# Kernel tuning notes

Measured on AMD Instinct MI355X. Metric: run time of the kernel, lower is better.

The kernel has to match this reference:

```python
import jax, jax.numpy as jnp
import numpy as np

B, NSL, DS = 8, 12, 768
L, R, DL = 24, 64, 4096
DP = 4096
DIM_T = NSL * 2 * DS          # 18432
FUSED = 1024 + 512            # 1536
GEN_IN = FUSED + 256 + 64     # 1856


def setup_inputs() -> dict:
    key = jax.random.key(0)
    ks = jax.random.split(key, 16)
    s = lambda d: 1.0 / np.sqrt(d)
    return {
        "A_small": jax.random.normal(ks[0], (B, NSL, 1, DS), jnp.float32),
        "B_small": jax.random.normal(ks[1], (B, NSL, DS, 1), jnp.float32),
        "prompt_emb": jax.random.normal(ks[2], (B, DP), jnp.float32),
        "W_ct": jax.random.normal(ks[3], (DIM_T, 1024), jnp.float32) * s(DIM_T),
        "b_ct": jnp.zeros((1024,), jnp.float32),
        "W_cp": jax.random.normal(ks[4], (DP, 512), jnp.float32) * s(DP),
        "b_cp": jnp.zeros((512,), jnp.float32),
        "W_pc": jax.random.normal(ks[5], (FUSED, L), jnp.float32) * s(FUSED),
        "b_pc": jnp.zeros((L,), jnp.float32),
        "E_layer": jax.random.normal(ks[6], (L, 256), jnp.float32),
        "E_chunk": jax.random.normal(ks[7], (R, 64), jnp.float32),
        "W_A": jax.random.normal(ks[8], (GEN_IN, DL), jnp.float32) * s(GEN_IN),
        "b_A": jnp.zeros((DL,), jnp.float32),
        "W_B": jax.random.normal(ks[9], (GEN_IN, DL), jnp.float32) * s(GEN_IN),
        "b_B": jnp.zeros((DL,), jnp.float32),
    }


def reference(A_small, B_small, prompt_emb, W_ct, b_ct, W_cp, b_cp, W_pc, b_pc,
              E_layer, E_chunk, W_A, b_A, W_B, b_B):
    bsz = prompt_emb.shape[0]
    flat_T = jnp.concatenate([A_small.reshape(bsz, -1), B_small.reshape(bsz, -1)], axis=-1)
    t_feat = jax.nn.relu(flat_T @ W_ct + b_ct)          # [B,1024]
    p_feat = jax.nn.relu(prompt_emb @ W_cp + b_cp)      # [B,512]
    fused = jnp.concatenate([t_feat, p_feat], axis=-1)  # [B,1536]
    logits = fused @ W_pc + b_pc                        # [B,L]
    y_soft = jax.nn.sigmoid(logits)                     # eval mode (no gumbel)
    y_hard = (y_soft > 0.5).astype(y_soft.dtype)
    gate = y_soft + jax.lax.stop_gradient(y_hard - y_soft)  # straight-through

    # Batched hypernetwork over all (layer, chunk) pairs instead of a double loop.
    ctx = jnp.broadcast_to(fused[:, None, None, :], (bsz, L, R, FUSED))
    le = jnp.broadcast_to(E_layer[None, :, None, :], (bsz, L, R, 256))
    ce = jnp.broadcast_to(E_chunk[None, None, :, :], (bsz, L, R, 64))
    gen = jnp.concatenate([ctx, le, ce], axis=-1)       # [B,L,R,1856]

    A = gen @ W_A + b_A                                 # [B,L,R,DL]
    Bm = gen @ W_B + b_B                                # [B,L,R,DL]
    A_large = A * gate[:, :, None, None]                # [B,L,R,DL]
    B_large = jnp.transpose(Bm, (0, 1, 3, 2))           # [B,L,DL,R]
    return (A_large, B_large, gate)
```

## Files before the change

kernel.cpp:

```cpp
#include <hip/hip_runtime.h>

typedef float v4f __attribute__((ext_vector_type(4)));

#define NB 8
#define NL 24
#define NR 64
#define ND 4096
#define NFUSED 1536
#define NTF 1024
#define NPF 512
#define KP 4096

#define FKC 12

#define WS_FACC  0
#define WS_GATE  49152
#define WS_PLA   49344
#define WS_PLB   245952
#define WS_CA    442560
#define WS_CBT   704704
#define WS_PFA   966848
#define WS_PFB   1360064

__global__ __launch_bounds__(256) void k_indep(
    const float* __restrict__ As, const float* __restrict__ Bs,
    const float* __restrict__ W_ct,
    const float* __restrict__ prompt, const float* __restrict__ W_cp,
    const float* __restrict__ E_layer, const float* __restrict__ E_chunk,
    const float* __restrict__ W_A, const float* __restrict__ W_B,
    float* __restrict__ fAcc,
    float* __restrict__ pLA, float* __restrict__ pLB,
    float* __restrict__ CA, float* __restrict__ CBT) {
  __shared__ float e[NR * 64];
  const int bx = blockIdx.x;
  const int tid = threadIdx.x;

  if (bx < 576) {
    const int j = (bx & 3) * 256 + tid;
    const int kc = bx >> 2;
    const int kbase = kc * 128;
    const float* xsrc = (kbase < 9216) ? (As + kbase) : (Bs + (kbase - 9216));
    {
      const int i0 = tid * 4;
      const int b = i0 >> 7, kk = i0 & 127;
      *(v4f*)&e[i0] = *(const v4f*)(xsrc + (size_t)b * 9216 + kk);
    }
    __syncthreads();
    float acc[NB] = {};
    for (int k4 = 0; k4 < 128; k4 += 4) {
      v4f xv[NB];
#pragma unroll
      for (int b = 0; b < NB; ++b) xv[b] = *(const v4f*)&e[b * 128 + k4];
#pragma unroll
      for (int u = 0; u < 4; ++u) {
        const float w = W_ct[(size_t)(kbase + k4 + u) * NTF + j];
#pragma unroll
        for (int b = 0; b < NB; ++b) acc[b] = fmaf(xv[b][u], w, acc[b]);
      }
    }
    const int rep = kc & 3;
#pragma unroll
    for (int b = 0; b < NB; ++b)
      atomicAdd(fAcc + (size_t)(rep * NB + b) * NFUSED + j, acc[b]);
  } else if (bx < 640) {
    const int t = bx - 576;
    const int j = (t & 1) * 256 + tid;
    const int kc = t >> 1;
    const int kbase = kc * 128;
    {
      const int i0 = tid * 4;
      const int b = i0 >> 7, kk = i0 & 127;
      *(v4f*)&e[i0] = *(const v4f*)(prompt + (size_t)b * KP + kbase + kk);
    }
    __syncthreads();
    float acc[NB] = {};
    for (int k4 = 0; k4 < 128; k4 += 4) {
      v4f xv[NB];
#pragma unroll
      for (int b = 0; b < NB; ++b) xv[b] = *(const v4f*)&e[b * 128 + k4];
#pragma unroll
      for (int u = 0; u < 4; ++u) {
        const float w = W_cp[(size_t)(kbase + k4 + u) * NPF + j];
#pragma unroll
        for (int b = 0; b < NB; ++b) acc[b] = fmaf(xv[b][u], w, acc[b]);
      }
    }
    const int rep = kc & 3;
#pragma unroll
    for (int b = 0; b < NB; ++b)
      atomicAdd(fAcc + (size_t)(rep * NB + b) * NFUSED + NTF + j, acc[b]);
  } else if (bx < 704) {
    const int t = bx - 640;
    const bool isA = t < 32;
    const int tt = isA ? t : t - 32;
    const int dc = tt & 15;
    const int kh = tt >> 4;
    const float* W = (isA ? W_A : W_B) + (size_t)(NFUSED + kh * 128) * ND;
    float* pL = (isA ? pLA : pLB) + (size_t)kh * NL * ND;
    const int d = dc * 256 + tid;
    float acc[NL] = {};
    for (int kk = 0; kk < 128; ++kk) {
      const float w = W[(size_t)kk * ND + d];
      const float* el = E_layer + kh * 128 + kk;
#pragma unroll
      for (int l = 0; l < NL; ++l) acc[l] = fmaf(el[l * 256], w, acc[l]);
    }
#pragma unroll
    for (int l = 0; l < NL; ++l) pL[(size_t)l * ND + d] = acc[l];
  } else {
    const int t = bx - 704;
    const bool isA = t < 16;
    const int tt = isA ? t : t - 16;
    const float* W = (isA ? W_A : W_B) + (size_t)(NFUSED + 256) * ND;
    for (int i = tid; i < NR * 64; i += 256) e[i] = E_chunk[i];
    __syncthreads();
    const int d = tt * 256 + tid;
    float w[64];
#pragma unroll
    for (int k = 0; k < 64; ++k) w[k] = W[(size_t)k * ND + d];
    for (int r = 0; r < NR; ++r) {
      float s = 0.f;
#pragma unroll
      for (int k = 0; k < 64; ++k) s = fmaf(e[r * 64 + k], w[k], s);
      if (isA) CA[(size_t)r * ND + d] = s;
      else     CBT[(size_t)d * NR + r] = s;
    }
  }
}

__global__ __launch_bounds__(256) void k_dep(
    const float* __restrict__ fAcc,
    const float* __restrict__ b_ct, const float* __restrict__ b_cp,
    const float* __restrict__ W_A, const float* __restrict__ W_B,
    const float* __restrict__ W_pc, const float* __restrict__ b_pc,
    float* __restrict__ pFA, float* __restrict__ pFB,
    float* __restrict__ gate_ws, float* __restrict__ gate_out) {
  __shared__ float sm[1664];
  const int bx = blockIdx.x;
  const int tid = threadIdx.x;

  if (bx < 384) {
    const bool isA = bx < 192;
    const int t = isA ? bx : bx - 192;
    const float* W = isA ? W_A : W_B;
    float* part = isA ? pFA : pFB;
    const int dc = t & 15;
    const int kc = t >> 4;
    const int kbase = kc * 128;

    for (int i = tid; i < 1024; i += 256) {
      const int b = i >> 7, kk = i & 127;
      const int k = kbase + kk;
      float v = (k < NTF) ? b_ct[k] : b_cp[k - NTF];
#pragma unroll
      for (int rep = 0; rep < 4; ++rep)
        v += fAcc[(size_t)(rep * NB + b) * NFUSED + k];
      sm[i] = fmaxf(v, 0.f);
    }
    __syncthreads();

    const int d = dc * 256 + tid;
    float acc[NB] = {};
    for (int kk = 0; kk < 128; ++kk) {
      const float w = W[(size_t)(kbase + kk) * ND + d];
#pragma unroll
      for (int b = 0; b < NB; ++b) acc[b] = fmaf(sm[b * 128 + kk], w, acc[b]);
    }
#pragma unroll
    for (int b = 0; b < NB; ++b)
      part[(size_t)(kc * NB + b) * ND + d] = acc[b];
  } else {
    const int b = bx - 384;
    for (int j = tid; j < NFUSED; j += 256) {
      float v = (j < NTF) ? b_ct[j] : b_cp[j - NTF];
#pragma unroll
      for (int rep = 0; rep < 4; ++rep)
        v += fAcc[(size_t)(rep * NB + b) * NFUSED + j];
      sm[j] = fmaxf(v, 0.f);
    }
    __syncthreads();
    float acc[NL] = {};
    for (int j = tid; j < NFUSED; j += 256) {
      const float f = sm[j];
#pragma unroll
      for (int l = 0; l < NL; ++l) acc[l] = fmaf(f, W_pc[j * NL + l], acc[l]);
    }
#pragma unroll
    for (int off = 32; off > 0; off >>= 1)
#pragma unroll
      for (int l = 0; l < NL; ++l) acc[l] += __shfl_down(acc[l], off);
    const int wave = tid >> 6, lane = tid & 63;
    if (lane == 0)
#pragma unroll
      for (int l = 0; l < NL; ++l) sm[NFUSED + wave * NL + l] = acc[l];
    __syncthreads();
    if (tid < NL) {
      float s = b_pc[tid];
#pragma unroll
      for (int w = 0; w < 4; ++w) s += sm[NFUSED + w * NL + tid];
      const float g = s > 0.f ? 1.f : 0.f;
      gate_ws[b * NL + tid] = g;
      gate_out[b * NL + tid] = g;
    }
  }
}

__global__ __launch_bounds__(256) void k_out(
    const float* __restrict__ pFA, const float* __restrict__ pFB,
    const float* __restrict__ b_A, const float* __restrict__ b_B,
    const float* __restrict__ pLA, const float* __restrict__ pLB,
    const float* __restrict__ CA, const float* __restrict__ CBT,
    const float* __restrict__ gate,
    float* __restrict__ outA, float* __restrict__ outB) {
  __shared__ float sbase[512];
  const int bx = blockIdx.x;
  const int tid = threadIdx.x;
  if (bx < 1536) {
    const int bl = bx >> 3;
    const int rest = bx & 7;
    const int b = bl / NL, l = bl % NL;
    const int d = (rest >> 1) * 1024 + tid * 4;
    const int r0 = (rest & 1) * 32;
    const float g = gate[bl];
    v4f base = *(const v4f*)(b_A + d);
#pragma unroll
    for (int kc = 0; kc < FKC; ++kc)
      base += *(const v4f*)(pFA + (size_t)(kc * NB + b) * ND + d);
    base += *(const v4f*)(pLA + (size_t)l * ND + d);
    base += *(const v4f*)(pLA + (size_t)(NL + l) * ND + d);
    float* outp = outA + ((size_t)bl * NR + r0) * ND + d;
#pragma unroll 4
    for (int r = 0; r < 32; ++r) {
      const v4f c = *(const v4f*)(CA + (size_t)(r0 + r) * ND + d);
      const v4f v = (base + c) * g;
      __builtin_nontemporal_store(v, (v4f*)outp);
      outp += ND;
    }
  } else {
    const int t = bx - 1536;
    const int bl = t >> 3;
    const int b = bl / NL, l = bl % NL;
    const int dbase = (t & 7) * 512;
    for (int dd = tid; dd < 512; dd += 256) {
      const int d = dbase + dd;
      float s = b_B[d] + pLB[(size_t)l * ND + d] + pLB[(size_t)(NL + l) * ND + d];
#pragma unroll
      for (int kc = 0; kc < FKC; ++kc)
        s += pFB[(size_t)(kc * NB + b) * ND + d];
      sbase[dd] = s;
    }
    __syncthreads();
    const int dd16 = tid >> 4;
    const int r4 = (tid & 15) * 4;
#pragma unroll 4
    for (int i = 0; i < 32; ++i) {
      const int dloc = i * 16 + dd16;
      const int d = dbase + dloc;
      const v4f c = *(const v4f*)(CBT + (size_t)d * NR + r4);
      const v4f v = c + sbase[dloc];
      __builtin_nontemporal_store(v, (v4f*)(outB + ((size_t)bl * ND + d) * NR + r4));
    }
  }
}

extern "C" void kernel_launch(void* const* d_in, const int* in_sizes, int n_in,
                              void* d_out, int out_size, void* d_ws, size_t ws_size,
                              hipStream_t stream) {
  const float* A_small   = (const float*)d_in[0];
  const float* B_small   = (const float*)d_in[1];
  const float* prompt    = (const float*)d_in[2];
  const float* W_ct      = (const float*)d_in[3];
  const float* b_ct      = (const float*)d_in[4];
  const float* W_cp      = (const float*)d_in[5];
  const float* b_cp      = (const float*)d_in[6];
  const float* W_pc      = (const float*)d_in[7];
  const float* b_pc      = (const float*)d_in[8];
  const float* E_layer   = (const float*)d_in[9];
  const float* E_chunk   = (const float*)d_in[10];
  const float* W_A       = (const float*)d_in[11];
  const float* b_A       = (const float*)d_in[12];
  const float* W_B       = (const float*)d_in[13];
  const float* b_B       = (const float*)d_in[14];

  float* ws    = (float*)d_ws;
  float* fAcc  = ws + WS_FACC;
  float* gatew = ws + WS_GATE;
  float* pLA   = ws + WS_PLA;
  float* pLB   = ws + WS_PLB;
  float* CA    = ws + WS_CA;
  float* CBT   = ws + WS_CBT;
  float* pFA   = ws + WS_PFA;
  float* pFB   = ws + WS_PFB;

  float* outA = (float*)d_out;
  float* outB = outA + (size_t)192 * NR * ND;
  float* outG = outB + (size_t)192 * ND * NR;

  hipMemsetAsync(fAcc, 0, (size_t)4 * NB * NFUSED * sizeof(float), stream);

  k_indep<<<736, 256, 0, stream>>>(A_small, B_small, W_ct, prompt, W_cp,
                                   E_layer, E_chunk, W_A, W_B,
                                   fAcc, pLA, pLB, CA, CBT);
  k_dep<<<392, 256, 0, stream>>>(fAcc, b_ct, b_cp, W_A, W_B,
                                 W_pc, b_pc, pFA, pFB, gatew, outG);
  k_out<<<3072, 256, 0, stream>>>(pFA, pFB, b_A, b_B, pLA, pLB, CA, CBT,
                                  gatew, outA, outG == nullptr ? nullptr : outB);
}
```

Measured before the change: 139.1 us.

## Fuse three kernels into one persistent kernel with grid-wide atomic barriers

Merges the independent-partials, dependent-projection, and output-expansion kernels into a single 1024-block kernel. Stages are separated by software grid barriers built on atomic counters in the workspace, which the memset now also zeroes. The aim is to remove kernel launch gaps and tail effects between stages. Workspace writes become nontemporal stores. The barriers assume all 1024 blocks are co-resident (launch bounds of 4 blocks per CU), otherwise the kernel deadlocks. Spin-waiting and the lower occupancy of a large persistent kernel may slow the bandwidth-bound output phase.

```diff
diff --git a/kernel.cpp b/kernel.cpp
--- a/kernel.cpp
+++ b/kernel.cpp
@@ -10,28 +10,48 @@
 #define NTF 1024
 #define NPF 512
 #define KP 4096
-
 #define FKC 12
-
-#define WS_FACC  0
-#define WS_GATE  49152
-#define WS_PLA   49344
-#define WS_PLB   245952
-#define WS_CA    442560
-#define WS_CBT   704704
-#define WS_PFA   966848
-#define WS_PFB   1360064
-
-__global__ __launch_bounds__(256) void k_indep(
+#define GRID 1024
+
+#define WS_CNT   0
+#define WS_FACC  64
+#define WS_GATE  49216
+#define WS_PLA   49408
+#define WS_PLB   246016
+#define WS_CA    442624
+#define WS_CBT   704768
+#define WS_PFA   966912
+#define WS_PFB   1360128
+#define WS_ZERO_N 49216
+
+__device__ __forceinline__ void nt(float v, float* p) {
+  __builtin_nontemporal_store(v, p);
+}
+
+__global__ __launch_bounds__(256, 4) void k_all(
     const float* __restrict__ As, const float* __restrict__ Bs,
     const float* __restrict__ W_ct,
     const float* __restrict__ prompt, const float* __restrict__ W_cp,
     const float* __restrict__ E_layer, const float* __restrict__ E_chunk,
     const float* __restrict__ W_A, const float* __restrict__ W_B,
-    float* __restrict__ fAcc,
-    float* __restrict__ pLA, float* __restrict__ pLB,
-    float* __restrict__ CA, float* __restrict__ CBT) {
-  __shared__ float e[NR * 64];
+    const float* __restrict__ b_ct, const float* __restrict__ b_cp,
+    const float* __restrict__ W_pc, const float* __restrict__ b_pc,
+    const float* __restrict__ b_A, const float* __restrict__ b_B,
+    float* __restrict__ ws,
+    float* __restrict__ outA, float* __restrict__ outB,
+    float* __restrict__ outG) {
+  __shared__ float sm[4096];
+  unsigned* cnt1 = (unsigned*)(ws + WS_CNT);
+  unsigned* cnt2 = (unsigned*)(ws + WS_CNT + 16);
+  float* fAcc = ws + WS_FACC;
+  float* gatew = ws + WS_GATE;
+  float* pLA = ws + WS_PLA;
+  float* pLB = ws + WS_PLB;
+  float* CA = ws + WS_CA;
+  float* CBT = ws + WS_CBT;
+  float* pFA = ws + WS_PFA;
+  float* pFB = ws + WS_PFB;
+
   const int bx = blockIdx.x;
   const int tid = threadIdx.x;
 
@@ -43,14 +63,14 @@
     {
       const int i0 = tid * 4;
       const int b = i0 >> 7, kk = i0 & 127;
-      *(v4f*)&e[i0] = *(const v4f*)(xsrc + (size_t)b * 9216 + kk);
+      *(v4f*)&sm[i0] = *(const v4f*)(xsrc + (size_t)b * 9216 + kk);
     }
     __syncthreads();
     float acc[NB] = {};
     for (int k4 = 0; k4 < 128; k4 += 4) {
       v4f xv[NB];
 #pragma unroll
-      for (int b = 0; b < NB; ++b) xv[b] = *(const v4f*)&e[b * 128 + k4];
+      for (int b = 0; b < NB; ++b) xv[b] = *(const v4f*)&sm[b * 128 + k4];
 #pragma unroll
       for (int u = 0; u < 4; ++u) {
         const float w = W_ct[(size_t)(kbase + k4 + u) * NTF + j];
@@ -70,14 +90,14 @@
     {
       const int i0 = tid * 4;
       const int b = i0 >> 7, kk = i0 & 127;
-      *(v4f*)&e[i0] = *(const v4f*)(prompt + (size_t)b * KP + kbase + kk);
+      *(v4f*)&sm[i0] = *(const v4f*)(prompt + (size_t)b * KP + kbase + kk);
     }
     __syncthreads();
     float acc[NB] = {};
     for (int k4 = 0; k4 < 128; k4 += 4) {
       v4f xv[NB];
 #pragma unroll
-      for (int b = 0; b < NB; ++b) xv[b] = *(const v4f*)&e[b * 128 + k4];
+      for (int b = 0; b < NB; ++b) xv[b] = *(const v4f*)&sm[b * 128 + k4];
 #pragma unroll
       for (int u = 0; u < 4; ++u) {
         const float w = W_cp[(size_t)(kbase + k4 + u) * NPF + j];
@@ -106,13 +126,13 @@
       for (int l = 0; l < NL; ++l) acc[l] = fmaf(el[l * 256], w, acc[l]);
     }
 #pragma unroll
-    for (int l = 0; l < NL; ++l) pL[(size_t)l * ND + d] = acc[l];
-  } else {
+    for (int l = 0; l < NL; ++l) nt(acc[l], pL + (size_t)l * ND + d);
+  } else if (bx < 736) {
     const int t = bx - 704;
     const bool isA = t < 16;
     const int tt = isA ? t : t - 16;
     const float* W = (isA ? W_A : W_B) + (size_t)(NFUSED + 256) * ND;
-    for (int i = tid; i < NR * 64; i += 256) e[i] = E_chunk[i];
+    for (int i = tid; i < NR * 64; i += 256) sm[i] = E_chunk[i];
     __syncthreads();
     const int d = tt * 256 + tid;
     float w[64];
@@ -121,144 +141,140 @@
     for (int r = 0; r < NR; ++r) {
       float s = 0.f;
 #pragma unroll
-      for (int k = 0; k < 64; ++k) s = fmaf(e[r * 64 + k], w[k], s);
-      if (isA) CA[(size_t)r * ND + d] = s;
-      else     CBT[(size_t)d * NR + r] = s;
+      for (int k = 0; k < 64; ++k) s = fmaf(sm[r * 64 + k], w[k], s);
+      if (isA) nt(s, CA + (size_t)r * ND + d);
+      else     nt(s, CBT + (size_t)d * NR + r);
     }
   }
-}
-
-__global__ __launch_bounds__(256) void k_dep(
-    const float* __restrict__ fAcc,
-    const float* __restrict__ b_ct, const float* __restrict__ b_cp,
-    const float* __restrict__ W_A, const float* __restrict__ W_B,
-    const float* __restrict__ W_pc, const float* __restrict__ b_pc,
-    float* __restrict__ pFA, float* __restrict__ pFB,
-    float* __restrict__ gate_ws, float* __restrict__ gate_out) {
-  __shared__ float sm[1664];
-  const int bx = blockIdx.x;
-  const int tid = threadIdx.x;
-
-  if (bx < 384) {
-    const bool isA = bx < 192;
-    const int t = isA ? bx : bx - 192;
-    const float* W = isA ? W_A : W_B;
-    float* part = isA ? pFA : pFB;
-    const int dc = t & 15;
-    const int kc = t >> 4;
-    const int kbase = kc * 128;
-
-    for (int i = tid; i < 1024; i += 256) {
-      const int b = i >> 7, kk = i & 127;
-      const int k = kbase + kk;
-      float v = (k < NTF) ? b_ct[k] : b_cp[k - NTF];
-#pragma unroll
-      for (int rep = 0; rep < 4; ++rep)
-        v += fAcc[(size_t)(rep * NB + b) * NFUSED + k];
-      sm[i] = fmaxf(v, 0.f);
+  __syncthreads();
+  if (tid == 0)
+    __hip_atomic_fetch_add(cnt1, 1u, __ATOMIC_RELEASE, __HIP_MEMORY_SCOPE_AGENT);
+
+  if (bx < 392) {
+    if (tid == 0) {
+      while (__hip_atomic_load(cnt1, __ATOMIC_RELAXED, __HIP_MEMORY_SCOPE_AGENT) < GRID)
+        __builtin_amdgcn_s_sleep(16);
     }
     __syncthreads();
-
-    const int d = dc * 256 + tid;
-    float acc[NB] = {};
-    for (int kk = 0; kk < 128; ++kk) {
-      const float w = W[(size_t)(kbase + kk) * ND + d];
-#pragma unroll
-      for (int b = 0; b < NB; ++b) acc[b] = fmaf(sm[b * 128 + kk], w, acc[b]);
-    }
-#pragma unroll
-    for (int b = 0; b < NB; ++b)
-      part[(size_t)(kc * NB + b) * ND + d] = acc[b];
-  } else {
-    const int b = bx - 384;
-    for (int j = tid; j < NFUSED; j += 256) {
-      float v = (j < NTF) ? b_ct[j] : b_cp[j - NTF];
-#pragma unroll
-      for (int rep = 0; rep < 4; ++rep)
-        v += fAcc[(size_t)(rep * NB + b) * NFUSED + j];
-      sm[j] = fmaxf(v, 0.f);
-    }
-    __syncthreads();
-    float acc[NL] = {};
-    for (int j = tid; j < NFUSED; j += 256) {
-      const float f = sm[j];
-#pragma unroll
-      for (int l = 0; l < NL; ++l) acc[l] = fmaf(f, W_pc[j * NL + l], acc[l]);
-    }
-#pragma unroll
-    for (int off = 32; off > 0; off >>= 1)
-#pragma unroll
-      for (int l = 0; l < NL; ++l) acc[l] += __shfl_down(acc[l], off);
-    const int wave = tid >> 6, lane = tid & 63;
-    if (lane == 0)
-#pragma unroll
-      for (int l = 0; l < NL; ++l) sm[NFUSED + wave * NL + l] = acc[l];
-    __syncthreads();
-    if (tid < NL) {
-      float s = b_pc[tid];
-#pragma unroll
-      for (int w = 0; w < 4; ++w) s += sm[NFUSED + w * NL + tid];
-      const float g = s > 0.f ? 1.f : 0.f;
-      gate_ws[b * NL + tid] = g;
-      gate_out[b * NL + tid] = g;
+    if (bx < 384) {
+      const bool isA = bx < 192;
+      const int t = isA ? bx : bx - 192;
+      const float* W = isA ? W_A : W_B;
+      float* part = isA ? pFA : pFB;
+      const int dc = t & 15;
+      const int kc = t >> 4;
+      const int kbase = kc * 128;
+      for (int i = tid; i < 1024; i += 256) {
+        const int b = i >> 7, kk = i & 127;
+        const int k = kbase + kk;
+        float v = (k < NTF) ? b_ct[k] : b_cp[k - NTF];
+#pragma unroll
+        for (int rep = 0; rep < 4; ++rep)
+          v += fAcc[(size_t)(rep * NB + b) * NFUSED + k];
+        sm[i] = fmaxf(v, 0.f);
+      }
+      __syncthreads();
+      const int d = dc * 256 + tid;
+      float acc[NB] = {};
+      for (int kk = 0; kk < 128; ++kk) {
+        const float w = W[(size_t)(kbase + kk) * ND + d];
+#pragma unroll
+        for (int b = 0; b < NB; ++b) acc[b] = fmaf(sm[b * 128 + kk], w, acc[b]);
+      }
+#pragma unroll
+      for (int b = 0; b < NB; ++b)
+        nt(acc[b], part + (size_t)(kc * NB + b) * ND + d);
+    } else {
+      const int b = bx - 384;
+      for (int j = tid; j < NFUSED; j += 256) {
+        float v = (j < NTF) ? b_ct[j] : b_cp[j - NTF];
+#pragma unroll
+        for (int rep = 0; rep < 4; ++rep)
+          v += fAcc[(size_t)(rep * NB + b) * NFUSED + j];
+        sm[j] = fmaxf(v, 0.f);
+      }
+      __syncthreads();
+      float acc[NL] = {};
+      for (int j = tid; j < NFUSED; j += 256) {
+        const float f = sm[j];
+#pragma unroll
+        for (int l = 0; l < NL; ++l) acc[l] = fmaf(f, W_pc[j * NL + l], acc[l]);
+      }
+#pragma unroll
+      for (int off = 32; off > 0; off >>= 1)
+#pragma unroll
+        for (int l = 0; l < NL; ++l) acc[l] += __shfl_down(acc[l], off);
+      const int wave = tid >> 6, lane = tid & 63;
+      if (lane == 0)
+#pragma unroll
+        for (int l = 0; l < NL; ++l) sm[NFUSED + wave * NL + l] = acc[l];
+      __syncthreads();
+      if (tid < NL) {
+        float s = b_pc[tid];
+#pragma unroll
+        for (int w = 0; w < 4; ++w) s += sm[NFUSED + w * NL + tid];
+        const float g = s > 0.f ? 1.f : 0.f;
+        nt(g, gatew + b * NL + tid);
+        nt(g, outG + b * NL + tid);
+      }
     }
   }
-}
-
-__global__ __launch_bounds__(256) void k_out(
-    const float* __restrict__ pFA, const float* __restrict__ pFB,
-    const float* __restrict__ b_A, const float* __restrict__ b_B,
-    const float* __restrict__ pLA, const float* __restrict__ pLB,
-    const float* __restrict__ CA, const float* __restrict__ CBT,
-    const float* __restrict__ gate,
-    float* __restrict__ outA, float* __restrict__ outB) {
-  __shared__ float sbase[512];
-  const int bx = blockIdx.x;
-  const int tid = threadIdx.x;
-  if (bx < 1536) {
-    const int bl = bx >> 3;
-    const int rest = bx & 7;
-    const int b = bl / NL, l = bl % NL;
-    const int d = (rest >> 1) * 1024 + tid * 4;
-    const int r0 = (rest & 1) * 32;
-    const float g = gate[bl];
-    v4f base = *(const v4f*)(b_A + d);
-#pragma unroll
-    for (int kc = 0; kc < FKC; ++kc)
-      base += *(const v4f*)(pFA + (size_t)(kc * NB + b) * ND + d);
-    base += *(const v4f*)(pLA + (size_t)l * ND + d);
-    base += *(const v4f*)(pLA + (size_t)(NL + l) * ND + d);
-    float* outp = outA + ((size_t)bl * NR + r0) * ND + d;
+  __syncthreads();
+  if (tid == 0)
+    __hip_atomic_fetch_add(cnt2, 1u, __ATOMIC_RELEASE, __HIP_MEMORY_SCOPE_AGENT);
+  if (tid == 0) {
+    while (__hip_atomic_load(cnt2, __ATOMIC_RELAXED, __HIP_MEMORY_SCOPE_AGENT) < GRID)
+      __builtin_amdgcn_s_sleep(16);
+  }
+  __syncthreads();
+
+  for (int u = bx; u < 3072; u += GRID) {
+    if (u < 1536) {
+      const int bl = u >> 3;
+      const int rest = u & 7;
+      const int b = bl / NL, l = bl % NL;
+      const int d = (rest >> 1) * 1024 + tid * 4;
+      const int r0 = (rest & 1) * 32;
+      const float g = gatew[bl];
+      v4f base = *(const v4f*)(b_A + d);
+#pragma unroll
+      for (int kc = 0; kc < FKC; ++kc)
+        base += *(const v4f*)(pFA + (size_t)(kc * NB + b) * ND + d);
+      base += *(const v4f*)(pLA + (size_t)l * ND + d);
+      base += *(const v4f*)(pLA + (size_t)(NL + l) * ND + d);
+      float* outp = outA + ((size_t)bl * NR + r0) * ND + d;
 #pragma unroll 4
-    for (int r = 0; r < 32; ++r) {
-      const v4f c = *(const v4f*)(CA + (size_t)(r0 + r) * ND + d);
-      const v4f v = (base + c) * g;
-      __builtin_nontemporal_store(v, (v4f*)outp);
-      outp += ND;
-    }
-  } else {
-    const int t = bx - 1536;
-    const int bl = t >> 3;
-    const int b = bl / NL, l = bl % NL;
-    const int dbase = (t & 7) * 512;
-    for (int dd = tid; dd < 512; dd += 256) {
-      const int d = dbase + dd;
-      float s = b_B[d] + pLB[(size_t)l * ND + d] + pLB[(size_t)(NL + l) * ND + d];
-#pragma unroll
-      for (int kc = 0; kc < FKC; ++kc)
-        s += pFB[(size_t)(kc * NB + b) * ND + d];
-      sbase[dd] = s;
-    }
-    __syncthreads();
-    const int dd16 = tid >> 4;
-    const int r4 = (tid & 15) * 4;
+      for (int r = 0; r < 32; ++r) {
+        const v4f c = *(const v4f*)(CA + (size_t)(r0 + r) * ND + d);
+        const v4f v = (base + c) * g;
+        __builtin_nontemporal_store(v, (v4f*)outp);
+        outp += ND;
+      }
+    } else {
+      const int t = u - 1536;
+      const int bl = t >> 3;
+      const int b = bl / NL, l = bl % NL;
+      const int dbase = (t & 7) * 512;
+      __syncthreads();
+      for (int dd = tid; dd < 512; dd += 256) {
+        const int d = dbase + dd;
+        float s = b_B[d] + pLB[(size_t)l * ND + d] + pLB[(size_t)(NL + l) * ND + d];
+#pragma unroll
+        for (int kc = 0; kc < FKC; ++kc)
+          s += pFB[(size_t)(kc * NB + b) * ND + d];
+        sm[dd] = s;
+      }
+      __syncthreads();
+      const int dd16 = tid >> 4;
+      const int r4 = (tid & 15) * 4;
 #pragma unroll 4
-    for (int i = 0; i < 32; ++i) {
-      const int dloc = i * 16 + dd16;
-      const int d = dbase + dloc;
-      const v4f c = *(const v4f*)(CBT + (size_t)d * NR + r4);
-      const v4f v = c + sbase[dloc];
-      __builtin_nontemporal_store(v, (v4f*)(outB + ((size_t)bl * ND + d) * NR + r4));
+      for (int i = 0; i < 32; ++i) {
+        const int dloc = i * 16 + dd16;
+        const int d = dbase + dloc;
+        const v4f c = *(const v4f*)(CBT + (size_t)d * NR + r4);
+        const v4f v = c + sm[dloc];
+        __builtin_nontemporal_store(v, (v4f*)(outB + ((size_t)bl * ND + d) * NR + r4));
+      }
     }
   }
 }
@@ -282,27 +298,15 @@
   const float* W_B       = (const float*)d_in[13];
   const float* b_B       = (const float*)d_in[14];
 
-  float* ws    = (float*)d_ws;
-  float* fAcc  = ws + WS_FACC;
-  float* gatew = ws + WS_GATE;
-  float* pLA   = ws + WS_PLA;
-  float* pLB   = ws + WS_PLB;
-  float* CA    = ws + WS_CA;
-  float* CBT   = ws + WS_CBT;
-  float* pFA   = ws + WS_PFA;
-  float* pFB   = ws + WS_PFB;
-
+  float* ws = (float*)d_ws;
   float* outA = (float*)d_out;
   float* outB = outA + (size_t)192 * NR * ND;
   float* outG = outB + (size_t)192 * ND * NR;
 
-  hipMemsetAsync(fAcc, 0, (size_t)4 * NB * NFUSED * sizeof(float), stream);
-
-  k_indep<<<736, 256, 0, stream>>>(A_small, B_small, W_ct, prompt, W_cp,
-                                   E_layer, E_chunk, W_A, W_B,
-                                   fAcc, pLA, pLB, CA, CBT);
-  k_dep<<<392, 256, 0, stream>>>(fAcc, b_ct, b_cp, W_A, W_B,
-                                 W_pc, b_pc, pFA, pFB, gatew, outG);
-  k_out<<<3072, 256, 0, stream>>>(pFA, pFB, b_A, b_B, pLA, pLB, CA, CBT,
-                                  gatew, outA, outG == nullptr ? nullptr : outB);
+  hipMemsetAsync(ws, 0, (size_t)WS_ZERO_N * sizeof(float), stream);
+
+  k_all<<<GRID, 256, 0, stream>>>(A_small, B_small, W_ct, prompt, W_cp,
+                                  E_layer, E_chunk, W_A, W_B,
+                                  b_ct, b_cp, W_pc, b_pc, b_A, b_B,
+                                  ws, outA, outB, outG);
 }
```

Result: slower. 308.1 us (+121.4%).
